# Performance work log

Measured on AMD Instinct MI355X. Metric: run time of the kernel, lower is better.

## Reference

```python
import jax, jax.numpy as jnp
import numpy as np

# ---- architecture constants (from init_kwargs) ----
BIG_K, SMALL_K = 51, 5
C_OUT, GROUP_IN = 96, 4
NK = -(-BIG_K // SMALL_K)          # 11 small kernels tile the big kernel
C_IN = C_OUT * NK                  # 1056
PADDING = SMALL_K - 1              # 4
EXTRA_PAD = PADDING - SMALL_K // 2 # 2
MID = BIG_K // 2                   # 25
REAL_PAD = [MID - i * SMALL_K - PADDING for i in range(NK)]
B, HOUT, WOUT = 8, 56, 56
HIN = HOUT + 2 * EXTRA_PAD         # 60


def setup_inputs() -> dict:
    key = jax.random.key(0)
    k1, k2, k3, k4 = jax.random.split(key, 4)
    rng = np.random.default_rng(0)
    rp = np.asarray(REAL_PAD, dtype=np.int32)
    # pad_hv: (C_IN, 2*GROUP_IN). Columns 0..G-1 horizontal shifts, G..2G-1 vertical.
    # For each (output-channel block, column) the nk channels get a random permutation of REAL_PAD.
    pad_hv = np.empty((C_IN, 2 * GROUP_IN), dtype=np.int32)
    for g in range(2 * GROUP_IN):
        for co in range(C_OUT):
            pad_hv[co * NK:(co + 1) * NK, g] = rng.permutation(rp)
    # idx_identit: (C_OUT, GROUP_IN); one randomly chosen channel inside each block.
    idx_identit = (rng.integers(0, NK, size=(C_OUT, GROUP_IN)) + np.arange(C_OUT)[:, None] * NK).astype(np.int32)
    x = jax.random.normal(k1, (B, C_IN, HIN, HIN), dtype=jnp.float32)
    w1 = jax.random.uniform(k2, (C_IN * GROUP_IN,), dtype=jnp.float32)
    w2 = jax.random.uniform(k3, (C_IN * GROUP_IN,), dtype=jnp.float32)
    w3 = jax.random.uniform(k4, (C_OUT * GROUP_IN,), dtype=jnp.float32)
    return {
        'x': x, 'w1': w1, 'w2': w2, 'w3': w3,
        'pad_hv': jnp.asarray(pad_hv), 'idx_identit': jnp.asarray(idx_identit),
        'b': B, 'hout': HOUT, 'wout': WOUT,
    }


def _forward(x, w1, w2, w3, pad_hv, idx_identit, hout, wout):
    Bx, C, H_in, W_in = x.shape
    c_out, G = idx_identit.shape
    nk = C // c_out
    ep = (H_in - hout) // 2  # extra_pad
    w1r = w1.reshape(G, C)
    w2r = w2.reshape(G, C)
    w3r = w3.reshape(G, c_out)

    # ---- horizontal shift branch (weights w1) ----
    xh = x[:, :, ep:ep + hout, :]                       # (B,C,hout,W_in)
    wpos = jnp.arange(wout)
    acc_h = jnp.zeros((Bx, C, hout, wout), x.dtype)
    for g in range(G):  # small fixed hyperparameter loop
        idxW = wpos[None, :] + ep + pad_hv[:, g][:, None]       # (C,wout)
        valid = (idxW >= 0) & (idxW < W_in)
        gat = jnp.take_along_axis(xh, jnp.clip(idxW, 0, W_in - 1)[None, :, None, :], axis=3)
        gat = jnp.where(valid[None, :, None, :], gat, 0.0)
        acc_h = acc_h + gat * w1r[g][None, :, None, None]
    out_h = acc_h.reshape(Bx, c_out, nk, hout, wout).sum(axis=2)  # scatter by idx_out (block structure)

    # ---- vertical shift branch (weights w2) ----
    xv = x[:, :, :, ep:ep + wout]                       # (B,C,H_in,wout)
    hpos = jnp.arange(hout)
    acc_v = jnp.zeros((Bx, C, hout, wout), x.dtype)
    for g in range(G):
        idxH = hpos[None, :] + ep + pad_hv[:, G + g][:, None]   # (C,hout)
        valid = (idxH >= 0) & (idxH < H_in)
        gat = jnp.take_along_axis(xv, jnp.clip(idxH, 0, H_in - 1)[None, :, :, None], axis=2)
        gat = jnp.where(valid[None, :, :, None], gat, 0.0)
        acc_v = acc_v + gat * w2r[g][None, :, None, None]
    out_v = acc_v.reshape(Bx, c_out, nk, hout, wout).sum(axis=2)

    # ---- identity branch (weights w3): pick one channel per output per group ----
    xc = x[:, :, ep:ep + hout, ep:ep + wout]            # (B,C,hout,wout)
    out_i = jnp.zeros((Bx, c_out, hout, wout), x.dtype)
    for g in range(G):
        out_i = out_i + xc[:, idx_identit[:, g]] * w3r[g][None, :, None, None]
    return out_h, out_v, out_i


def reference(x, w1, w2, w3, pad_hv, idx_identit, b, hout, wout):
    # Matches AddShift_mp_linear_module.forward: returns the three chunks (x, y, z)
    return _forward(x, w1, w2, w3, pad_hv, idx_identit, hout, wout)
```

## Files before the change

kernel.cpp:

```cpp
#include <hip/hip_runtime.h>

#define BATCH   8
#define C_OUT_N 96
#define NK      11
#define C_IN_N  1056
#define GRP     4
#define HOUT    56
#define WOUT    56
#define HIN     60
#define WIN     60
#define EP      2

#define RPAD    27
#define CPADL   28
#define STRIDE  108
#define RTOT    106
#define TILE_DW (RTOT * STRIDE)

__global__ __launch_bounds__(256, 3) void addshift_kernel(
    const float* __restrict__ x,
    const float* __restrict__ w1,
    const float* __restrict__ w2,
    const float* __restrict__ w3,
    const int*   __restrict__ pad_hv,
    const int*   __restrict__ idx_identit,
    float* __restrict__ out)
{
    const int co = blockIdx.x;
    const int b  = blockIdx.y;
    const int tid = threadIdx.x;

    __shared__ __align__(16) float tile[TILE_DW];

    {
        const float4 z4 = {0.f, 0.f, 0.f, 0.f};
        for (int j = tid; j < TILE_DW / 4; j += 256)
            ((float4*)tile)[j] = z4;
    }

    const int h0 = (tid >> 6) * 14;
    const int w  = tid & 63;
    const int wc = (w < WOUT) ? w : (WOUT - 1);

    int   kI[GRP];
    float w3v[GRP];
#pragma unroll
    for (int g = 0; g < GRP; ++g) {
        kI[g]  = idx_identit[co * GRP + g] - co * NK;
        w3v[g] = w3[g * C_OUT_N + co];
    }

    float accH[14], accV[14], accI[14];
#pragma unroll
    for (int i = 0; i < 14; ++i) { accH[i] = 0.f; accV[i] = 0.f; accI[i] = 0.f; }

    const float* chan_base = x + ((size_t)b * C_IN_N + (size_t)co * NK) * (HIN * WIN);

    float4 pre[4];
    {
        const float4* src4 = (const float4*)chan_base;
#pragma unroll
        for (int t = 0; t < 4; ++t) {
            int j = tid + t * 256;
            pre[t] = src4[j < 900 ? j : 899];
        }
    }

    __syncthreads();

    const int rowH = (h0 + EP + RPAD) * STRIDE;
    const int colV = wc + EP + CPADL;

#pragma unroll 1
    for (int k = 0; k < NK; ++k) {
#pragma unroll
        for (int t = 0; t < 4; ++t) {
            int j = tid + t * 256;
            if (j < 900) {
                int row = j / 15;
                int c4  = j - row * 15;
                *(float4*)&tile[(row + RPAD) * STRIDE + CPADL + c4 * 4] = pre[t];
            }
        }
        __syncthreads();

        if (k < NK - 1) {
            const float4* src4 = (const float4*)(chan_base + (size_t)(k + 1) * (HIN * WIN));
#pragma unroll
            for (int t = 0; t < 4; ++t) {
                int j = tid + t * 256;
                pre[t] = src4[j < 900 ? j : 899];
            }
        }

        const int c = co * NK + k;
        int ph[GRP], pv[GRP];
        float a1[GRP], a2[GRP];
#pragma unroll
        for (int g = 0; g < GRP; ++g) {
            ph[g] = pad_hv[c * 8 + g];
            pv[g] = pad_hv[c * 8 + 4 + g];
            a1[g] = w1[g * C_IN_N + c];
            a2[g] = w2[g * C_IN_N + c];
        }
        float wi = 0.f;
#pragma unroll
        for (int g = 0; g < GRP; ++g)
            if (kI[g] == k) wi += w3v[g];

#pragma unroll
        for (int g = 0; g < GRP; ++g) {
            const int offH = rowH + colV + ph[g];
            const int offV = (h0 + EP + pv[g] + RPAD) * STRIDE + colV;
#pragma unroll
            for (int i = 0; i < 14; ++i) {
                accH[i] = fmaf(tile[offH + i * STRIDE], a1[g], accH[i]);
                accV[i] = fmaf(tile[offV + i * STRIDE], a2[g], accV[i]);
            }
        }
        if (wi != 0.f) {
            const int offI = rowH + colV;
#pragma unroll
            for (int i = 0; i < 14; ++i)
                accI[i] = fmaf(tile[offI + i * STRIDE], wi, accI[i]);
        }
        __syncthreads();
    }

    if (w < WOUT) {
        const size_t OSZ = (size_t)BATCH * C_OUT_N * HOUT * WOUT;
        const size_t base = (((size_t)b * C_OUT_N + co) * HOUT + h0) * WOUT + w;
#pragma unroll
        for (int i = 0; i < 14; ++i) {
            out[base + (size_t)i * WOUT]            = accH[i];
            out[OSZ + base + (size_t)i * WOUT]      = accV[i];
            out[2 * OSZ + base + (size_t)i * WOUT]  = accI[i];
        }
    }
}

extern "C" void kernel_launch(void* const* d_in, const int* in_sizes, int n_in,
                              void* d_out, int out_size, void* d_ws, size_t ws_size,
                              hipStream_t stream) {
    const float* x   = (const float*)d_in[0];
    const float* w1  = (const float*)d_in[1];
    const float* w2  = (const float*)d_in[2];
    const float* w3  = (const float*)d_in[3];
    const int* pad_hv      = (const int*)d_in[4];
    const int* idx_identit = (const int*)d_in[5];
    float* out = (float*)d_out;

    dim3 grid(C_OUT_N, BATCH);
    dim3 block(256);
    addshift_kernel<<<grid, block, 0, stream>>>(x, w1, w2, w3, pad_hv, idx_identit, out);
}
```

Baseline: 239.8 us.

## Transpose LDS tile column-major, double block size, stage nontemporal vector output stores

Stores each input channel in shared memory transposed (column-major with stride 107) and drops column padding, using per-column bounds masking for horizontal shifts instead. Blocks grow to 512 threads, each computing 7 rows instead of 14, and the input is prefetched as scalar loads rather than float4. Outputs are staged through LDS and written as coalesced float4 nontemporal stores. This aims to raise occupancy and coalesce stores, at the cost of scalar global loads and transposed LDS writes that may cause bank conflicts.

```diff
diff --git a/kernel.cpp b/kernel.cpp
--- a/kernel.cpp
+++ b/kernel.cpp
@@ -12,12 +12,13 @@
 #define EP      2
 
 #define RPAD    27
-#define CPADL   28
-#define STRIDE  108
-#define RTOT    106
-#define TILE_DW (RTOT * STRIDE)
+#define TSTR    107
+#define TILE_DW (WIN * TSTR)
+#define NELEM   (HIN * WIN)
 
-__global__ __launch_bounds__(256, 3) void addshift_kernel(
+typedef float fvec4 __attribute__((ext_vector_type(4)));
+
+__global__ __launch_bounds__(512, 6) void addshift_kernel(
     const float* __restrict__ x,
     const float* __restrict__ w1,
     const float* __restrict__ w2,
@@ -26,21 +27,22 @@
     const int*   __restrict__ idx_identit,
     float* __restrict__ out)
 {
-    const int co = blockIdx.x;
-    const int b  = blockIdx.y;
+    const int co  = blockIdx.x;
+    const int b   = blockIdx.y;
     const int tid = threadIdx.x;
+    const int wv  = tid >> 6;
+    const int w   = tid & 63;
 
     __shared__ __align__(16) float tile[TILE_DW];
 
     {
-        const float4 z4 = {0.f, 0.f, 0.f, 0.f};
-        for (int j = tid; j < TILE_DW / 4; j += 256)
-            ((float4*)tile)[j] = z4;
+        const fvec4 z4 = {0.f, 0.f, 0.f, 0.f};
+#pragma unroll
+        for (int t = 0; t < 4; ++t) {
+            int j = tid + t * 512;
+            if (j < TILE_DW / 4) ((fvec4*)tile)[j] = z4;
+        }
     }
-
-    const int h0 = (tid >> 6) * 14;
-    const int w  = tid & 63;
-    const int wc = (w < WOUT) ? w : (WOUT - 1);
 
     int   kI[GRP];
     float w3v[GRP];
@@ -50,46 +52,45 @@
         w3v[g] = w3[g * C_OUT_N + co];
     }
 
-    float accH[14], accV[14], accI[14];
+    float accH[7], accV[7], accI[7];
 #pragma unroll
-    for (int i = 0; i < 14; ++i) { accH[i] = 0.f; accV[i] = 0.f; accI[i] = 0.f; }
+    for (int i = 0; i < 7; ++i) { accH[i] = 0.f; accV[i] = 0.f; accI[i] = 0.f; }
 
-    const float* chan_base = x + ((size_t)b * C_IN_N + (size_t)co * NK) * (HIN * WIN);
+    const float* chan_base = x + ((size_t)b * C_IN_N + (size_t)co * NK) * NELEM;
 
-    float4 pre[4];
-    {
-        const float4* src4 = (const float4*)chan_base;
+    float pre[8];
 #pragma unroll
-        for (int t = 0; t < 4; ++t) {
-            int j = tid + t * 256;
-            pre[t] = src4[j < 900 ? j : 899];
-        }
+    for (int t = 0; t < 8; ++t) {
+        int idx = tid + t * 512;
+        pre[t] = chan_base[idx < NELEM ? idx : NELEM - 1];
     }
 
     __syncthreads();
 
-    const int rowH = (h0 + EP + RPAD) * STRIDE;
-    const int colV = wc + EP + CPADL;
+    const int h0   = wv * 7;
+    const int colV = (w + EP < WIN) ? (w + EP) : (WIN - 1);
+    const int baseVcol = colV * TSTR;
+    const int rowB = h0 + EP + RPAD;
 
 #pragma unroll 1
     for (int k = 0; k < NK; ++k) {
 #pragma unroll
-        for (int t = 0; t < 4; ++t) {
-            int j = tid + t * 256;
-            if (j < 900) {
-                int row = j / 15;
-                int c4  = j - row * 15;
-                *(float4*)&tile[(row + RPAD) * STRIDE + CPADL + c4 * 4] = pre[t];
+        for (int t = 0; t < 8; ++t) {
+            int idx = tid + t * 512;
+            if (idx < NELEM) {
+                int row = idx / WIN;
+                int col = idx - row * WIN;
+                tile[col * TSTR + row + RPAD] = pre[t];
             }
         }
         __syncthreads();
 
         if (k < NK - 1) {
-            const float4* src4 = (const float4*)(chan_base + (size_t)(k + 1) * (HIN * WIN));
+            const float* nxt = chan_base + (size_t)(k + 1) * NELEM;
 #pragma unroll
-            for (int t = 0; t < 4; ++t) {
-                int j = tid + t * 256;
-                pre[t] = src4[j < 900 ? j : 899];
+            for (int t = 0; t < 8; ++t) {
+                int idx = tid + t * 512;
+                pre[t] = nxt[idx < NELEM ? idx : NELEM - 1];
             }
         }
 
@@ -110,32 +111,53 @@
 
 #pragma unroll
         for (int g = 0; g < GRP; ++g) {
-            const int offH = rowH + colV + ph[g];
-            const int offV = (h0 + EP + pv[g] + RPAD) * STRIDE + colV;
+            const int iw = w + EP + ph[g];
+            const bool vH = (unsigned)iw < (unsigned)WIN;
+            const int colH = vH ? iw : 0;
+            const float a1m = vH ? a1[g] : 0.f;
+            const int offH = colH * TSTR + rowB;
+            const int offV = baseVcol + rowB + pv[g];
 #pragma unroll
-            for (int i = 0; i < 14; ++i) {
-                accH[i] = fmaf(tile[offH + i * STRIDE], a1[g], accH[i]);
-                accV[i] = fmaf(tile[offV + i * STRIDE], a2[g], accV[i]);
+            for (int i = 0; i < 7; ++i) {
+                accH[i] = fmaf(tile[offH + i], a1m, accH[i]);
+                accV[i] = fmaf(tile[offV + i], a2[g], accV[i]);
             }
         }
         if (wi != 0.f) {
-            const int offI = rowH + colV;
+            const int offI = baseVcol + rowB;
 #pragma unroll
-            for (int i = 0; i < 14; ++i)
-                accI[i] = fmaf(tile[offI + i * STRIDE], wi, accI[i]);
+            for (int i = 0; i < 7; ++i)
+                accI[i] = fmaf(tile[offI + i], wi, accI[i]);
         }
         __syncthreads();
     }
 
-    if (w < WOUT) {
-        const size_t OSZ = (size_t)BATCH * C_OUT_N * HOUT * WOUT;
-        const size_t base = (((size_t)b * C_OUT_N + co) * HOUT + h0) * WOUT + w;
+    const size_t OSZ  = (size_t)BATCH * C_OUT_N * HOUT * WOUT;
+    const size_t rbase = (((size_t)b * C_OUT_N + co) * HOUT + h0) * WOUT;
+    const int ebase = wv * (7 * WOUT);
+
+    float* outs[3] = { out + rbase, out + OSZ + rbase, out + 2 * OSZ + rbase };
+    const float* accs[3] = { accH, accV, accI };
+
 #pragma unroll
-        for (int i = 0; i < 14; ++i) {
-            out[base + (size_t)i * WOUT]            = accH[i];
-            out[OSZ + base + (size_t)i * WOUT]      = accV[i];
-            out[2 * OSZ + base + (size_t)i * WOUT]  = accI[i];
+    for (int o = 0; o < 3; ++o) {
+        const float* a = accs[o];
+        if (w < WOUT) {
+#pragma unroll
+            for (int i = 0; i < 7; ++i)
+                tile[ebase + i * WOUT + w] = a[i];
         }
+        __syncthreads();
+#pragma unroll
+        for (int j = 0; j < 2; ++j) {
+            int idx = w + j * 64;
+            if (idx < 98) {
+                const float* p = &tile[ebase + idx * 4];
+                fvec4 v = { p[0], p[1], p[2], p[3] };
+                __builtin_nontemporal_store(v, (fvec4*)(outs[o] + idx * 4));
+            }
+        }
+        __syncthreads();
     }
 }
 
@@ -151,6 +173,6 @@
     float* out = (float*)d_out;
 
     dim3 grid(C_OUT_N, BATCH);
-    dim3 block(256);
+    dim3 block(512);
     addshift_kernel<<<grid, block, 0, stream>>>(x, w1, w2, w3, pad_hv, idx_identit, out);
 }
```

Result: slower. 291.3 us (+21.5%).
